# Kernel tuning notes

Hardware: AMD Instinct MI355X
Metric: run time of the kernel (lower is better)

The kernel has to match this reference:

```python
import jax, jax.numpy as jnp
import numpy as np

TOP_K = 90
TEMP = 0.04
EPS_LN = 1e-5

def _l2norm(x):
    n = jnp.linalg.norm(x, axis=-1, keepdims=True)
    return x / jnp.maximum(n, 1e-12)

def _layernorm(x, g, b):
    mu = jnp.mean(x, axis=-1, keepdims=True)
    var = jnp.mean((x - mu) ** 2, axis=-1, keepdims=True)
    return (x - mu) * jax.lax.rsqrt(var + EPS_LN) * g + b

def setup_inputs() -> dict:
    key = jax.random.key(0)
    ks = jax.random.split(key, 8)
    B, N, D, ES = 2048, 100000, 1024, 101
    H1, H2 = 256, 128
    inp = {
        "en_1024": jax.random.normal(ks[0], (B, D), jnp.float32),
        "en_db": jax.random.normal(ks[1], (N, D), jnp.float32),
        "es_db": jax.random.normal(ks[2], (N, D), jnp.float32),
        "sp_idx": jax.random.randint(ks[3], (ES,), 0, D),
        "W1": jax.random.normal(ks[4], (D + ES, H1), jnp.float32) * 0.02,
        "b1": jnp.zeros((H1,), jnp.float32),
        "g1": jnp.ones((H1,), jnp.float32),
        "be1": jnp.zeros((H1,), jnp.float32),
        "W2": jax.random.normal(ks[5], (H1, H2), jnp.float32) * 0.02,
        "b2": jnp.zeros((H2,), jnp.float32),
        "g2": jnp.ones((H2,), jnp.float32),
        "be2": jnp.zeros((H2,), jnp.float32),
        "W3": jax.random.normal(ks[6], (H2, ES), jnp.float32) * 0.02,
        "b3": jnp.zeros((ES,), jnp.float32),
    }
    return inp

def reference(en_1024, en_db, es_db, sp_idx, W1, b1, g1, be1, W2, b2, g2, be2, W3, b3):
    # --- retrieval: cosine sim + topk softmax + weighted gather-sum ---
    q = _l2norm(en_1024)            # (B, 1024)
    db = _l2norm(en_db)             # (N, 1024)
    sims = q @ db.T                 # (B, N)
    top_sims, top_idx = jax.lax.top_k(sims, TOP_K)      # (B, K)
    w = jax.nn.softmax(top_sims / TEMP, axis=-1)        # (B, K)
    gathered = es_db[top_idx]       # (B, K, 1024)
    es_retrieved_1024 = jnp.einsum('bk,bkd->bd', w, gathered)  # (B, 1024)
    es_retrieved_101 = es_retrieved_1024[:, sp_idx]     # (B, 101)
    # --- fusion MLP (residual correction) ---
    feat = jnp.concatenate([en_1024, es_retrieved_101], axis=-1)  # (B, 1125)
    h = jax.nn.gelu(_layernorm(feat @ W1 + b1, g1, be1), approximate=False)
    h = jax.nn.gelu(_layernorm(h @ W2 + b2, g2, be2), approximate=False)
    delta = h @ W3 + b3
    es_pred_101 = es_retrieved_101 + delta
    return (es_pred_101, es_retrieved_101, delta)
```

## Files before the change

kernel.cpp:

```cpp
#include <hip/hip_runtime.h>
#include <hip/hip_bf16.h>
#include <hip/hip_fp16.h>

typedef int i32x4 __attribute__((ext_vector_type(4)));
typedef float f32x4 __attribute__((ext_vector_type(4)));

#define B_ROWS 2048
#define N_DB   100000
#define D_DIM  1024
#define ES     101
#define H1D    256
#define H2D    128
#define TOPK   90
#define TKEEP  128
#define TEMPV  0.04f
#define NTOT   100352
#define NT_ALL 392
#define ESS    104
#define CAP    1024
#define CNTS   16
#define RCAP   24
#define GTHR   0.085f

#define GLOAD16(g, l) __builtin_amdgcn_global_load_lds( \
    (const __attribute__((address_space(1))) unsigned int*)(g), \
    (__attribute__((address_space(3))) unsigned int*)(l), 16, 0, 0)

__device__ inline int q8clamp(float x) {
  int q = (int)rintf(x);
  return q < -127 ? -127 : (q > 127 ? 127 : q);
}

__global__ __launch_bounds__(256) void qnorm_kernel(const float* __restrict__ en,
                                                    char* __restrict__ qa,
                                                    float* __restrict__ fa) {
  __shared__ float red[4], redm[4];
  int b = blockIdx.x, t = threadIdx.x;
  float4 v = ((const float4*)(en + (size_t)b * D_DIM))[t];
  float ss = v.x * v.x + v.y * v.y + v.z * v.z + v.w * v.w;
  float mx = fmaxf(fmaxf(fabsf(v.x), fabsf(v.y)), fmaxf(fabsf(v.z), fabsf(v.w)));
  for (int o = 32; o; o >>= 1) { ss += __shfl_xor(ss, o); mx = fmaxf(mx, __shfl_xor(mx, o)); }
  if ((t & 63) == 0) { red[t >> 6] = ss; redm[t >> 6] = mx; }
  __syncthreads();
  float tot = red[0] + red[1] + red[2] + red[3];
  float mtot = fmaxf(fmaxf(redm[0], redm[1]), fmaxf(redm[2], redm[3]));
  float s = fmaxf(mtot, 1e-30f) / 127.0f;
  float rs = 1.0f / s;
  if (t == 0) fa[b] = s / fmaxf(sqrtf(tot), 1e-12f);
  int packed = (q8clamp(v.x * rs) & 0xff) | ((q8clamp(v.y * rs) & 0xff) << 8) |
               ((q8clamp(v.z * rs) & 0xff) << 16) | ((q8clamp(v.w * rs) & 0xff) << 24);
  ((int*)(qa + (size_t)b * D_DIM))[t] = packed;
}

__global__ __launch_bounds__(256) void prep_kernel(const float* __restrict__ db,
                                                   char* __restrict__ qb,
                                                   float* __restrict__ fb,
                                                   const float* __restrict__ es,
                                                   const int* __restrict__ sp,
                                                   float* __restrict__ es_sub) {
  __shared__ float red[4], redm[4];
  __shared__ float row[1024];
  __shared__ int sps[ES];
  int r = blockIdx.x, t = threadIdx.x;
  if (r >= N_DB) {
    ((int*)(qb + (size_t)r * D_DIM))[t] = 0;
    if (t == 0) fb[r] = 0.f;
    return;
  }
  float4 v = ((const float4*)(db + (size_t)r * D_DIM))[t];
  float ss = v.x * v.x + v.y * v.y + v.z * v.z + v.w * v.w;
  float mx = fmaxf(fmaxf(fabsf(v.x), fabsf(v.y)), fmaxf(fabsf(v.z), fabsf(v.w)));
  for (int o = 32; o; o >>= 1) { ss += __shfl_xor(ss, o); mx = fmaxf(mx, __shfl_xor(mx, o)); }
  if ((t & 63) == 0) { red[t >> 6] = ss; redm[t >> 6] = mx; }
  if (t < ES) sps[t] = sp[t];
  ((float4*)row)[t] = ((const float4*)(es + (size_t)r * D_DIM))[t];
  __syncthreads();
  float tot = red[0] + red[1] + red[2] + red[3];
  float mtot = fmaxf(fmaxf(redm[0], redm[1]), fmaxf(redm[2], redm[3]));
  float s = fmaxf(mtot, 1e-30f) / 127.0f;
  float rs = 1.0f / s;
  if (t == 0) fb[r] = s / fmaxf(sqrtf(tot), 1e-12f);
  int packed = (q8clamp(v.x * rs) & 0xff) | ((q8clamp(v.y * rs) & 0xff) << 8) |
               ((q8clamp(v.z * rs) & 0xff) << 16) | ((q8clamp(v.w * rs) & 0xff) << 24);
  ((int*)(qb + (size_t)r * D_DIM))[t] = packed;
  if (t < ES) es_sub[(size_t)r * ESS + t] = row[sps[t]];
}

__global__ __launch_bounds__(512) void gemm_kernel(const char* __restrict__ qa,
                                                   const char* __restrict__ qb,
                                                   const float* __restrict__ fav,
                                                   const float* __restrict__ fbv,
                                                   float* __restrict__ cand_v,
                                                   int* __restrict__ cand_i,
                                                   int* __restrict__ cand_cnt) {
  __shared__ char shmem[52224];
  char* Bs = shmem;
  int t = threadIdx.x;
  int lane = t & 63, wid = t >> 6;
  int wr = wid >> 2, wc = wid & 3;
  int l15 = lane & 15, l4 = lane >> 4;
  int id = blockIdx.x;
  int swz = (id & 7) * (gridDim.x >> 3) + (id >> 3);
  int bm = swz & 7, bn = swz >> 3;
  int m0 = bm * 256;
  int col0 = bn * 256;

  const char* srcB[4];
  int dstoff[4];
  #pragma unroll
  for (int i = 0; i < 4; ++i) {
    int L = i * 512 + t;
    int row = L >> 3;
    int colb = ((L & 7) * 16) ^ ((row & 7) << 4);
    srcB[i] = qb + (size_t)(col0 + row) * D_DIM + colb;
    dstoff[i] = L * 16;
  }
  const char* aptr[8];
  #pragma unroll
  for (int f = 0; f < 8; ++f)
    aptr[f] = qa + (size_t)(m0 + wr * 128 + f * 16 + l15) * D_DIM + l4 * 16;

  i32x4 acc[8][4] = {};

  for (int kt = 0; kt < D_DIM; kt += 128) {
    #pragma unroll
    for (int i = 0; i < 4; ++i) GLOAD16(srcB[i] + kt, Bs + dstoff[i]);
    i32x4 a[8][2];
    #pragma unroll
    for (int f = 0; f < 8; ++f)
      #pragma unroll
      for (int s = 0; s < 2; ++s)
        a[f][s] = *(const i32x4*)(aptr[f] + kt + s * 64);
    __syncthreads();
    #pragma unroll
    for (int s = 0; s < 2; ++s) {
      i32x4 b[4];
      #pragma unroll
      for (int f = 0; f < 4; ++f) {
        int rowB = wc * 64 + f * 16 + l15;
        int offB = rowB * 128 + ((s * 64 + l4 * 16) ^ ((rowB & 7) << 4));
        b[f] = *(const i32x4*)(Bs + offB);
      }
      #pragma unroll
      for (int fm = 0; fm < 8; ++fm)
        #pragma unroll
        for (int fn = 0; fn < 4; ++fn)
          acc[fm][fn] = __builtin_amdgcn_mfma_i32_16x16x64_i8(a[fm][s], b[fn], acc[fm][fn], 0, 0, 0);
    }
    __syncthreads();
  }

  float*    fa_l = (float*)shmem;
  float*    fb_l = (float*)(shmem + 1024);
  unsigned* rcnt = (unsigned*)(shmem + 2048);
  float*    rvv  = (float*)(shmem + 3072);
  int*      rvi  = (int*)(shmem + 27648);
  if (t < 256) {
    fa_l[t] = fav[m0 + t];
    fb_l[t] = (col0 + t < N_DB) ? fbv[col0 + t] : 0.f;
    rcnt[t] = 0;
  }
  __syncthreads();
  #pragma unroll
  for (int fm = 0; fm < 8; ++fm)
    #pragma unroll
    for (int fn = 0; fn < 4; ++fn) {
      int ncl = wc * 64 + fn * 16 + l15;
      int gcol = col0 + ncl;
      if (gcol >= N_DB) continue;
      float fbn = fb_l[ncl];
      #pragma unroll
      for (int r = 0; r < 4; ++r) {
        int lrow = wr * 128 + fm * 16 + l4 * 4 + r;
        float v = (float)acc[fm][fn][r] * fa_l[lrow] * fbn;
        if (v > GTHR) {
          unsigned p = atomicAdd(&rcnt[lrow], 1u);
          if (p < RCAP) { rvv[lrow * RCAP + p] = v; rvi[lrow * RCAP + p] = gcol; }
        }
      }
    }
  __syncthreads();
  if (t < 256) {
    unsigned k = rcnt[t]; if (k > RCAP) k = RCAP;
    if (k) {
      int m = m0 + t;
      int base = atomicAdd(&cand_cnt[(size_t)m * CNTS], (int)k);
      for (unsigned j = 0; j < k; ++j) {
        int p = base + (int)j;
        if (p < CAP) {
          cand_v[(size_t)m * CAP + p] = rvv[t * RCAP + j];
          cand_i[(size_t)m * CAP + p] = rvi[t * RCAP + j];
        }
      }
    }
  }
}

__device__ inline void bsort(float* cv, int* ci, int t, int cnt, int p2) {
  for (int i = t; i < p2; i += 256)
    if (i >= cnt) { cv[i] = -3e38f; ci[i] = 0x7fffffff; }
  for (int k = 2; k <= p2; k <<= 1)
    for (int j = k >> 1; j > 0; j >>= 1) {
      __syncthreads();
      for (int i = t; i < p2; i += 256) {
        int ixj = i ^ j;
        if (ixj > i) {
          float v1 = cv[i], v2 = cv[ixj];
          int i1 = ci[i], i2 = ci[ixj];
          bool aBeforeB = (v1 > v2) || (v1 == v2 && i1 < i2);
          bool dirAsc = (i & k) != 0;
          bool doSwap = dirAsc ? aBeforeB : !aBeforeB;
          if (doSwap) { cv[i] = v2; cv[ixj] = v1; ci[i] = i2; ci[ixj] = i1; }
        }
      }
    }
  __syncthreads();
}

__global__ __launch_bounds__(256) void topk_final_kernel(const float* __restrict__ cand_v,
                                                         const int* __restrict__ cand_i,
                                                         const int* __restrict__ cand_cnt,
                                                         float* __restrict__ sval,
                                                         int* __restrict__ sidx) {
  __shared__ float cv[CAP];
  __shared__ int   ci[CAP];
  int b = blockIdx.x, t = threadIdx.x;
  int nc = cand_cnt[(size_t)b * CNTS]; if (nc > CAP) nc = CAP;
  for (int i = t; i < nc; i += 256) {
    cv[i] = cand_v[(size_t)b * CAP + i];
    ci[i] = cand_i[(size_t)b * CAP + i];
  }
  __syncthreads();
  int p2 = 128; while (p2 < nc) p2 <<= 1;
  bsort(cv, ci, t, nc, p2);
  if (t < TKEEP) { sval[(size_t)b * TKEEP + t] = cv[t]; sidx[(size_t)b * TKEEP + t] = ci[t]; }
}

__global__ __launch_bounds__(256) void rescore_kernel(const float* __restrict__ en,
                                                      const float* __restrict__ db,
                                                      float* __restrict__ sval,
                                                      int* __restrict__ sidx) {
  __shared__ float qs[1024];
  __shared__ double wred[4];
  __shared__ float cv[TKEEP];
  __shared__ int   ci[TKEEP];
  int b = blockIdx.x, t = threadIdx.x;
  int lane = t & 63, wid = t >> 6;
  double nq2 = 0.0;
  for (int i = t; i < 1024; i += 256) {
    float v = en[(size_t)b * D_DIM + i];
    qs[i] = v;
    nq2 = fma((double)v, (double)v, nq2);
  }
  for (int o = 32; o; o >>= 1) nq2 += __shfl_xor(nq2, o);
  if (lane == 0) wred[wid] = nq2;
  __syncthreads();
  double nq2t = wred[0] + wred[1] + wred[2] + wred[3];
  double nq = sqrt(nq2t); if (nq < 1e-12) nq = 1e-12;
  const f32x4* qs4 = (const f32x4*)qs;
  for (int c = wid * 32; c < wid * 32 + 32; ++c) {
    int idx = sidx[(size_t)b * TKEEP + c];
    if (idx < 0 || idx >= N_DB) idx = 0;
    const f32x4* dr4 = (const f32x4*)(db + (size_t)idx * D_DIM);
    double dot = 0.0, nd2 = 0.0;
    #pragma unroll
    for (int j = 0; j < 4; ++j) {
      f32x4 d = dr4[lane + j * 64];
      f32x4 q = qs4[lane + j * 64];
      #pragma unroll
      for (int e = 0; e < 4; ++e) {
        dot = fma((double)q[e], (double)d[e], dot);
        nd2 = fma((double)d[e], (double)d[e], nd2);
      }
    }
    for (int o = 32; o; o >>= 1) { dot += __shfl_xor(dot, o); nd2 += __shfl_xor(nd2, o); }
    if (lane == 0) {
      double nd = sqrt(nd2); if (nd < 1e-12) nd = 1e-12;
      cv[c] = (float)(dot / (nq * nd));
      ci[c] = idx;
    }
  }
  __syncthreads();
  bsort(cv, ci, t, TKEEP, TKEEP);
  if (t < TKEEP) {
    sval[(size_t)b * TKEEP + t] = cv[t];
    sidx[(size_t)b * TKEEP + t] = ci[t];
  }
}

__global__ __launch_bounds__(128) void softgather_kernel(const float* __restrict__ sval,
                                                         const int* __restrict__ sidx,
                                                         const float* __restrict__ es_sub,
                                                         float* __restrict__ esr,
                                                         float* __restrict__ out_esr) {
  __shared__ float w[TOPK];
  __shared__ int id[TOPK];
  __shared__ float ssum;
  int b = blockIdx.x, t = threadIdx.x;
  if (t < TOPK) {
    float vmax = sval[(size_t)b * TKEEP];
    w[t] = expf((sval[(size_t)b * TKEEP + t] - vmax) / TEMPV);
    id[t] = sidx[(size_t)b * TKEEP + t];
  }
  __syncthreads();
  if (t == 0) {
    float s = 0.f;
    for (int k = 0; k < TOPK; ++k) s += w[k];
    ssum = s;
  }
  __syncthreads();
  float inv = 1.0f / ssum;
  if (t < ES) {
    float acc = 0.f;
    for (int k = 0; k < TOPK; ++k) acc += w[k] * es_sub[(size_t)id[k] * ESS + t];
    acc *= inv;
    esr[b * ES + t] = acc;
    out_esr[b * ES + t] = acc;
  }
}

__global__ __launch_bounds__(256) void mlp_kernel(const float* __restrict__ en,
                                                  const float* __restrict__ esr,
                                                  const float* __restrict__ W1, const float* __restrict__ b1,
                                                  const float* __restrict__ g1, const float* __restrict__ be1,
                                                  const float* __restrict__ W2, const float* __restrict__ b2,
                                                  const float* __restrict__ g2, const float* __restrict__ be2,
                                                  const float* __restrict__ W3, const float* __restrict__ b3,
                                                  float* __restrict__ out) {
  __shared__ float feat[8][1128];
  __shared__ float h1s[8][H1D];
  __shared__ float h2s[8][H2D];
  int t = threadIdx.x;
  int b0 = blockIdx.x * 8;
  int wid = t >> 6, lane = t & 63;
  for (int r = 0; r < 8; ++r) {
    const float* src = en + (size_t)(b0 + r) * D_DIM;
    for (int i = t; i < 1024; i += 256) feat[r][i] = src[i];
    if (t < ES) feat[r][1024 + t] = esr[(b0 + r) * ES + t];
  }
  __syncthreads();
  float acc[8];
  #pragma unroll
  for (int r = 0; r < 8; ++r) acc[r] = b1[t];
  for (int k = 0; k < 1125; ++k) {
    float wv = W1[k * H1D + t];
    #pragma unroll
    for (int r = 0; r < 8; ++r) acc[r] += feat[r][k] * wv;
  }
  #pragma unroll
  for (int r = 0; r < 8; ++r) h1s[r][t] = acc[r];
  __syncthreads();
  for (int rr = 0; rr < 2; ++rr) {
    int r = wid + rr * 4;
    float s = 0.f, s2 = 0.f;
    for (int j = lane; j < H1D; j += 64) { float x = h1s[r][j]; s += x; s2 += x * x; }
    for (int o = 32; o; o >>= 1) { s += __shfl_xor(s, o); s2 += __shfl_xor(s2, o); }
    float mu = s / H1D, var = s2 / H1D - mu * mu, rs = rsqrtf(var + 1e-5f);
    for (int j = lane; j < H1D; j += 64) {
      float x = (h1s[r][j] - mu) * rs * g1[j] + be1[j];
      h1s[r][j] = 0.5f * x * (1.0f + erff(x * 0.70710678118654752f));
    }
  }
  __syncthreads();
  if (t < H2D) {
    float acc2[8];
    #pragma unroll
    for (int r = 0; r < 8; ++r) acc2[r] = b2[t];
    for (int k = 0; k < H1D; ++k) {
      float wv = W2[k * H2D + t];
      #pragma unroll
      for (int r = 0; r < 8; ++r) acc2[r] += h1s[r][k] * wv;
    }
    #pragma unroll
    for (int r = 0; r < 8; ++r) h2s[r][t] = acc2[r];
  }
  __syncthreads();
  for (int rr = 0; rr < 2; ++rr) {
    int r = wid + rr * 4;
    float s = 0.f, s2 = 0.f;
    for (int j = lane; j < H2D; j += 64) { float x = h2s[r][j]; s += x; s2 += x * x; }
    for (int o = 32; o; o >>= 1) { s += __shfl_xor(s, o); s2 += __shfl_xor(s2, o); }
    float mu = s / H2D, var = s2 / H2D - mu * mu, rs = rsqrtf(var + 1e-5f);
    for (int j = lane; j < H2D; j += 64) {
      float x = (h2s[r][j] - mu) * rs * g2[j] + be2[j];
      h2s[r][j] = 0.5f * x * (1.0f + erff(x * 0.70710678118654752f));
    }
  }
  __syncthreads();
  if (t < ES) {
    for (int r = 0; r < 8; ++r) {
      float a = b3[t];
      for (int k = 0; k < H2D; ++k) a += h2s[r][k] * W3[k * ES + t];
      float ev = esr[(b0 + r) * ES + t];
      out[(size_t)(b0 + r) * ES + t] = ev + a;
      out[2 * (size_t)B_ROWS * ES + (size_t)(b0 + r) * ES + t] = a;
    }
  }
}

extern "C" void kernel_launch(void* const* d_in, const int* in_sizes, int n_in,
                              void* d_out, int out_size, void* d_ws, size_t ws_size,
                              hipStream_t stream) {
  const float* en   = (const float*)d_in[0];
  const float* endb = (const float*)d_in[1];
  const float* esdb = (const float*)d_in[2];
  const int*   sp   = (const int*)d_in[3];
  const float* W1   = (const float*)d_in[4];
  const float* b1   = (const float*)d_in[5];
  const float* g1   = (const float*)d_in[6];
  const float* be1  = (const float*)d_in[7];
  const float* W2   = (const float*)d_in[8];
  const float* b2   = (const float*)d_in[9];
  const float* g2   = (const float*)d_in[10];
  const float* be2  = (const float*)d_in[11];
  const float* W3   = (const float*)d_in[12];
  const float* b3   = (const float*)d_in[13];
  float* out = (float*)d_out;

  char* ws = (char*)d_ws;
  size_t off = 0;
  auto alloc = [&](size_t bytes) -> void* {
    void* p = ws + off;
    off += (bytes + 255) & ~(size_t)255;
    return p;
  };
  char*  qa     = (char*) alloc((size_t)B_ROWS * D_DIM);
  char*  qb     = (char*) alloc((size_t)NTOT * D_DIM);
  float* fa     = (float*)alloc((size_t)B_ROWS * sizeof(float));
  float* fb     = (float*)alloc((size_t)NTOT * sizeof(float));
  float* sval   = (float*)alloc((size_t)B_ROWS * TKEEP * sizeof(float));
  int*   sidx   = (int*)  alloc((size_t)B_ROWS * TKEEP * sizeof(int));
  float* cand_v = (float*)alloc((size_t)B_ROWS * CAP * sizeof(float));
  int*   cand_i = (int*)  alloc((size_t)B_ROWS * CAP * sizeof(int));
  int*   cand_cnt = (int*)alloc((size_t)B_ROWS * CNTS * sizeof(int));
  float* es_sub = (float*)alloc((size_t)N_DB * ESS * sizeof(float));
  float* esr    = (float*)alloc((size_t)B_ROWS * ES * sizeof(float));
  (void)ws_size; (void)in_sizes; (void)n_in; (void)out_size;

  hipMemsetAsync(cand_cnt, 0, (size_t)B_ROWS * CNTS * sizeof(int), stream);
  hipLaunchKernelGGL(qnorm_kernel, dim3(B_ROWS), dim3(256), 0, stream, en, qa, fa);
  hipLaunchKernelGGL(prep_kernel, dim3(NTOT), dim3(256), 0, stream, endb, qb, fb, esdb, sp, es_sub);
  hipLaunchKernelGGL(gemm_kernel, dim3(NT_ALL * 8), dim3(512), 0, stream,
                     qa, qb, fa, fb, cand_v, cand_i, cand_cnt);
  hipLaunchKernelGGL(topk_final_kernel, dim3(B_ROWS), dim3(256), 0, stream,
                     cand_v, cand_i, cand_cnt, sval, sidx);
  hipLaunchKernelGGL(rescore_kernel, dim3(B_ROWS), dim3(256), 0, stream, en, endb, sval, sidx);
  hipLaunchKernelGGL(softgather_kernel, dim3(B_ROWS), dim3(128), 0, stream,
                     sval, sidx, es_sub, esr, out + (size_t)B_ROWS * ES);
  hipLaunchKernelGGL(mlp_kernel, dim3(B_ROWS / 8), dim3(256), 0, stream,
                     en, esr, W1, b1, g1, be1, W2, b2, g2, be2, W3, b3, out);
}
```

Baseline: 1.173 ms.

## Pre-tile quantized queries for coalesced GEMM A loads and fuse select/rescore/gather

A new kernel rearranges the int8 query matrix into an MFMA-fragment-ordered layout, so each wavefront's A-operand loads in the GEMM become contiguous 1 KB chunks instead of strided row reads. The A loads are also issued before the B global-to-LDS copies. The top-k selection, fp64 rescoring and softmax gather kernels are merged into one per-row kernel, which removes the sval/sidx round trips and two launches. The cost is an extra small transpose kernel and higher shared-memory use in the fused kernel.

```diff
diff --git a/kernel.cpp b/kernel.cpp
--- a/kernel.cpp
+++ b/kernel.cpp
@@ -52,6 +52,15 @@
   ((int*)(qa + (size_t)b * D_DIM))[t] = packed;
 }
 
+__global__ __launch_bounds__(64) void qat_kernel(const char* __restrict__ qa,
+                                                 char* __restrict__ qaT) {
+  int m = blockIdx.x, c = threadIdx.x;
+  int kb = c >> 3, s = (c >> 2) & 1, l4 = c & 3;
+  int g = m >> 4, l15 = m & 15;
+  const int4 v = *(const int4*)(qa + (size_t)m * D_DIM + c * 16);
+  *(int4*)(qaT + (size_t)g * 16384 + kb * 2048 + s * 1024 + l15 * 64 + l4 * 16) = v;
+}
+
 __global__ __launch_bounds__(256) void prep_kernel(const float* __restrict__ db,
                                                    char* __restrict__ qb,
                                                    float* __restrict__ fb,
@@ -86,7 +95,7 @@
   if (t < ES) es_sub[(size_t)r * ESS + t] = row[sps[t]];
 }
 
-__global__ __launch_bounds__(512) void gemm_kernel(const char* __restrict__ qa,
+__global__ __launch_bounds__(512) void gemm_kernel(const char* __restrict__ qaT,
                                                    const char* __restrict__ qb,
                                                    const float* __restrict__ fav,
                                                    const float* __restrict__ fbv,
@@ -116,21 +125,23 @@
     dstoff[i] = L * 16;
   }
   const char* aptr[8];
+  int aoff = l15 * 64 + l4 * 16;
   #pragma unroll
   for (int f = 0; f < 8; ++f)
-    aptr[f] = qa + (size_t)(m0 + wr * 128 + f * 16 + l15) * D_DIM + l4 * 16;
+    aptr[f] = qaT + (size_t)(bm * 16 + wr * 8 + f) * 16384 + aoff;
 
   i32x4 acc[8][4] = {};
 
   for (int kt = 0; kt < D_DIM; kt += 128) {
+    int kb2 = (kt >> 7) * 2048;
+    i32x4 a[8][2];
+    #pragma unroll
+    for (int f = 0; f < 8; ++f) {
+      a[f][0] = *(const i32x4*)(aptr[f] + kb2);
+      a[f][1] = *(const i32x4*)(aptr[f] + kb2 + 1024);
+    }
     #pragma unroll
     for (int i = 0; i < 4; ++i) GLOAD16(srcB[i] + kt, Bs + dstoff[i]);
-    i32x4 a[8][2];
-    #pragma unroll
-    for (int f = 0; f < 8; ++f)
-      #pragma unroll
-      for (int s = 0; s < 2; ++s)
-        a[f][s] = *(const i32x4*)(aptr[f] + kt + s * 64);
     __syncthreads();
     #pragma unroll
     for (int s = 0; s < 2; ++s) {
@@ -217,35 +228,27 @@
   __syncthreads();
 }
 
-__global__ __launch_bounds__(256) void topk_final_kernel(const float* __restrict__ cand_v,
-                                                         const int* __restrict__ cand_i,
-                                                         const int* __restrict__ cand_cnt,
-                                                         float* __restrict__ sval,
-                                                         int* __restrict__ sidx) {
+__global__ __launch_bounds__(256) void select_rescore_kernel(const float* __restrict__ cand_v,
+                                                             const int* __restrict__ cand_i,
+                                                             const int* __restrict__ cand_cnt,
+                                                             const float* __restrict__ en,
+                                                             const float* __restrict__ db,
+                                                             const float* __restrict__ es_sub,
+                                                             float* __restrict__ esr,
+                                                             float* __restrict__ out_esr) {
   __shared__ float cv[CAP];
   __shared__ int   ci[CAP];
+  __shared__ float qs[1024];
+  __shared__ double wred[4];
+  __shared__ float w[TOPK];
+  __shared__ float ssum;
   int b = blockIdx.x, t = threadIdx.x;
+  int lane = t & 63, wid = t >> 6;
   int nc = cand_cnt[(size_t)b * CNTS]; if (nc > CAP) nc = CAP;
   for (int i = t; i < nc; i += 256) {
     cv[i] = cand_v[(size_t)b * CAP + i];
     ci[i] = cand_i[(size_t)b * CAP + i];
   }
-  __syncthreads();
-  int p2 = 128; while (p2 < nc) p2 <<= 1;
-  bsort(cv, ci, t, nc, p2);
-  if (t < TKEEP) { sval[(size_t)b * TKEEP + t] = cv[t]; sidx[(size_t)b * TKEEP + t] = ci[t]; }
-}
-
-__global__ __launch_bounds__(256) void rescore_kernel(const float* __restrict__ en,
-                                                      const float* __restrict__ db,
-                                                      float* __restrict__ sval,
-                                                      int* __restrict__ sidx) {
-  __shared__ float qs[1024];
-  __shared__ double wred[4];
-  __shared__ float cv[TKEEP];
-  __shared__ int   ci[TKEEP];
-  int b = blockIdx.x, t = threadIdx.x;
-  int lane = t & 63, wid = t >> 6;
   double nq2 = 0.0;
   for (int i = t; i < 1024; i += 256) {
     float v = en[(size_t)b * D_DIM + i];
@@ -255,11 +258,13 @@
   for (int o = 32; o; o >>= 1) nq2 += __shfl_xor(nq2, o);
   if (lane == 0) wred[wid] = nq2;
   __syncthreads();
+  int p2 = 128; while (p2 < nc) p2 <<= 1;
+  bsort(cv, ci, t, nc, p2);
   double nq2t = wred[0] + wred[1] + wred[2] + wred[3];
   double nq = sqrt(nq2t); if (nq < 1e-12) nq = 1e-12;
   const f32x4* qs4 = (const f32x4*)qs;
   for (int c = wid * 32; c < wid * 32 + 32; ++c) {
-    int idx = sidx[(size_t)b * TKEEP + c];
+    int idx = ci[c];
     if (idx < 0 || idx >= N_DB) idx = 0;
     const f32x4* dr4 = (const f32x4*)(db + (size_t)idx * D_DIM);
     double dot = 0.0, nd2 = 0.0;
@@ -282,26 +287,7 @@
   }
   __syncthreads();
   bsort(cv, ci, t, TKEEP, TKEEP);
-  if (t < TKEEP) {
-    sval[(size_t)b * TKEEP + t] = cv[t];
-    sidx[(size_t)b * TKEEP + t] = ci[t];
-  }
-}
-
-__global__ __launch_bounds__(128) void softgather_kernel(const float* __restrict__ sval,
-                                                         const int* __restrict__ sidx,
-                                                         const float* __restrict__ es_sub,
-                                                         float* __restrict__ esr,
-                                                         float* __restrict__ out_esr) {
-  __shared__ float w[TOPK];
-  __shared__ int id[TOPK];
-  __shared__ float ssum;
-  int b = blockIdx.x, t = threadIdx.x;
-  if (t < TOPK) {
-    float vmax = sval[(size_t)b * TKEEP];
-    w[t] = expf((sval[(size_t)b * TKEEP + t] - vmax) / TEMPV);
-    id[t] = sidx[(size_t)b * TKEEP + t];
-  }
+  if (t < TOPK) w[t] = expf((cv[t] - cv[0]) / TEMPV);
   __syncthreads();
   if (t == 0) {
     float s = 0.f;
@@ -312,7 +298,7 @@
   float inv = 1.0f / ssum;
   if (t < ES) {
     float acc = 0.f;
-    for (int k = 0; k < TOPK; ++k) acc += w[k] * es_sub[(size_t)id[k] * ESS + t];
+    for (int k = 0; k < TOPK; ++k) acc += w[k] * es_sub[(size_t)ci[k] * ESS + t];
     acc *= inv;
     esr[b * ES + t] = acc;
     out_esr[b * ES + t] = acc;
@@ -425,11 +411,10 @@
     return p;
   };
   char*  qa     = (char*) alloc((size_t)B_ROWS * D_DIM);
+  char*  qaT    = (char*) alloc((size_t)B_ROWS * D_DIM);
   char*  qb     = (char*) alloc((size_t)NTOT * D_DIM);
   float* fa     = (float*)alloc((size_t)B_ROWS * sizeof(float));
   float* fb     = (float*)alloc((size_t)NTOT * sizeof(float));
-  float* sval   = (float*)alloc((size_t)B_ROWS * TKEEP * sizeof(float));
-  int*   sidx   = (int*)  alloc((size_t)B_ROWS * TKEEP * sizeof(int));
   float* cand_v = (float*)alloc((size_t)B_ROWS * CAP * sizeof(float));
   int*   cand_i = (int*)  alloc((size_t)B_ROWS * CAP * sizeof(int));
   int*   cand_cnt = (int*)alloc((size_t)B_ROWS * CNTS * sizeof(int));
@@ -439,14 +424,13 @@
 
   hipMemsetAsync(cand_cnt, 0, (size_t)B_ROWS * CNTS * sizeof(int), stream);
   hipLaunchKernelGGL(qnorm_kernel, dim3(B_ROWS), dim3(256), 0, stream, en, qa, fa);
+  hipLaunchKernelGGL(qat_kernel, dim3(B_ROWS), dim3(64), 0, stream, qa, qaT);
   hipLaunchKernelGGL(prep_kernel, dim3(NTOT), dim3(256), 0, stream, endb, qb, fb, esdb, sp, es_sub);
   hipLaunchKernelGGL(gemm_kernel, dim3(NT_ALL * 8), dim3(512), 0, stream,
-                     qa, qb, fa, fb, cand_v, cand_i, cand_cnt);
-  hipLaunchKernelGGL(topk_final_kernel, dim3(B_ROWS), dim3(256), 0, stream,
-                     cand_v, cand_i, cand_cnt, sval, sidx);
-  hipLaunchKernelGGL(rescore_kernel, dim3(B_ROWS), dim3(256), 0, stream, en, endb, sval, sidx);
-  hipLaunchKernelGGL(softgather_kernel, dim3(B_ROWS), dim3(128), 0, stream,
-                     sval, sidx, es_sub, esr, out + (size_t)B_ROWS * ES);
+                     qaT, qb, fa, fb, cand_v, cand_i, cand_cnt);
+  hipLaunchKernelGGL(select_rescore_kernel, dim3(B_ROWS), dim3(256), 0, stream,
+                     cand_v, cand_i, cand_cnt, en, endb, es_sub,
+                     esr, out + (size_t)B_ROWS * ES);
   hipLaunchKernelGGL(mlp_kernel, dim3(B_ROWS / 8), dim3(256), 0, stream,
                      en, esr, W1, b1, g1, be1, W2, b2, g2, be2, W3, b3, out);
 }
```

Result: faster. 1.003 ms (-14.4%).
